# Kernel tuning notes

Measured on AMD Instinct MI355X. Metric: run time of the kernel, lower is better.

## Reference

```python
import jax, jax.numpy as jnp
import numpy as np

E = 8      # n_routed_experts (== n_local)
K = 2      # n_activated_experts (top-k)
DIM = 2048
INTER = 1408
N_SHARED = 2
STD = 0.02


def setup_inputs() -> dict:
    key = jax.random.key(0)
    ks = jax.random.split(key, 9)
    B, S = 2, 2048
    return {
        "x": jax.random.normal(ks[0], (B, S, DIM), dtype=jnp.float32),
        "gate_w": jax.random.normal(ks[1], (E, DIM), dtype=jnp.float32) * STD,
        "router_bias": jnp.zeros((E,), dtype=jnp.float32),
        "W1": jax.random.normal(ks[2], (E, DIM, INTER), dtype=jnp.float32) * STD,
        "W3": jax.random.normal(ks[3], (E, DIM, INTER), dtype=jnp.float32) * STD,
        "W2": jax.random.normal(ks[4], (E, INTER, DIM), dtype=jnp.float32) * STD,
        "sw1": jax.random.normal(ks[5], (N_SHARED * INTER, DIM), dtype=jnp.float32) * STD,
        "sw3": jax.random.normal(ks[6], (N_SHARED * INTER, DIM), dtype=jnp.float32) * STD,
        "sw2": jax.random.normal(ks[7], (DIM, N_SHARED * INTER), dtype=jnp.float32) * STD,
    }


def reference(x, gate_w, router_bias, W1, W3, W2, sw1, sw3, sw2):
    B, S, D = x.shape
    X = x.reshape(-1, D)                       # [T, D]
    T = X.shape[0]

    # ---- Router: sigmoid scores, biased top-k selection, normalized weights
    logits = jnp.einsum('td,ed->te', X, gate_w)          # [T, E] (route_scale == 1.0)
    scores = jax.nn.sigmoid(logits)
    sel = scores + router_bias[None, :]
    _, idx = jax.lax.top_k(sel, K)                       # [T, K] int indices
    w = jnp.take_along_axis(scores, idx, axis=1)         # gather true scores
    w = w / jnp.clip(jnp.sum(w, axis=-1, keepdims=True), 1e-12)

    # Dense combine matrix [T, E]: gate weight where expert selected else 0
    gate_full = jnp.zeros((T, E), dtype=w.dtype).at[jnp.arange(T)[:, None], idx].set(w)

    # ---- Expert MLPs (SwiGLU) computed per-expert, combined by routing weight
    h1 = jnp.einsum('td,edh->eth', X, W1)                # [E, T, INTER]
    h3 = jnp.einsum('td,edh->eth', X, W3)
    y = jnp.einsum('eth,ehd->etd', jax.nn.silu(h1) * h3, W2)  # [E, T, D]
    out = jnp.einsum('etd,te->td', y, gate_full)         # weighted combine

    # ---- Shared expert MLP (always on)
    shared = jnp.einsum('th,dh->td',
                        jax.nn.silu(jnp.einsum('td,hd->th', X, sw1))
                        * jnp.einsum('td,hd->th', X, sw3), sw2)
    out = out + shared
    return out.reshape(B, S, D)
```

## Files before the change

### kernel.cpp

```cpp
#include <hip/hip_runtime.h>

#define DEV __device__ __forceinline__

typedef __attribute__((ext_vector_type(8))) short short8;
typedef __attribute__((ext_vector_type(4))) float floatx4;

constexpr int Tn  = 4096;
constexpr int Dm  = 2048;
constexpr int In  = 1408;
constexpr int En  = 8;
constexpr int SIn = 2816;
constexpr int CAP = 10240;

constexpr int RT_H = (CAP / 256) * (In / 128);
constexpr int SH_H = (Tn / 256) * (SIn / 128);
constexpr int RT_O = (CAP / 256) * (Dm / 256);
constexpr int SH_O = (Tn / 256) * (Dm / 256);

DEV unsigned short f2bf(float f) {
  unsigned int u = __float_as_uint(f);
  u += 0x7FFF + ((u >> 16) & 1);
  return (unsigned short)(u >> 16);
}

DEV float bf2f(unsigned short u) {
  return __uint_as_float(((unsigned int)u) << 16);
}

DEV void stg(const char* g, char* l) {
  __builtin_amdgcn_global_load_lds(
      (const __attribute__((address_space(1))) unsigned int*)g,
      (__attribute__((address_space(3))) unsigned int*)l, 16, 0, 0);
}

DEV unsigned ldsoff(const void* p) {
  return (unsigned)(unsigned long long)(__attribute__((address_space(3))) const char*)p;
}

#define BARR()  __builtin_amdgcn_s_barrier()
#define LGKM0() do { asm volatile("s_waitcnt lgkmcnt(0)" ::: "memory"); \
                     __builtin_amdgcn_sched_barrier(0); } while (0)
#define LGKM8() asm volatile("s_waitcnt lgkmcnt(8)" ::: "memory")
#define VMC(n)  asm volatile("s_waitcnt vmcnt(" #n ")" ::: "memory")
#define PRIO(x) __builtin_amdgcn_s_setprio(x)

#define DSR(dst, addr, OFFSTR) \
  asm volatile("ds_read_b128 %0, %1 offset:" OFFSTR : "=v"(dst) : "v"(addr))

#define RDA_LO(af, a) do { \
  DSR(af[0][0], a, "0");     DSR(af[0][1], a, "1024"); \
  DSR(af[1][0], a, "2048");  DSR(af[1][1], a, "3072"); \
  DSR(af[2][0], a, "4096");  DSR(af[2][1], a, "5120"); \
  DSR(af[3][0], a, "6144");  DSR(af[3][1], a, "7168"); } while (0)
#define RDA_HI(af, a) do { \
  DSR(af[0][0], a, "8192");  DSR(af[0][1], a, "9216"); \
  DSR(af[1][0], a, "10240"); DSR(af[1][1], a, "11264"); \
  DSR(af[2][0], a, "12288"); DSR(af[2][1], a, "13312"); \
  DSR(af[3][0], a, "14336"); DSR(af[3][1], a, "15360"); } while (0)
#define RDB_LO(bf, a) do { \
  DSR(bf[0][0], a, "0");    DSR(bf[0][1], a, "1024"); \
  DSR(bf[1][0], a, "2048"); DSR(bf[1][1], a, "3072"); } while (0)
#define RDB_HI(bf, a) do { \
  DSR(bf[2][0], a, "4096"); DSR(bf[2][1], a, "5120"); \
  DSR(bf[3][0], a, "6144"); DSR(bf[3][1], a, "7168"); } while (0)


__global__ void convert_all_kernel(const float* __restrict__ x,
                                   const float* __restrict__ sw1,
                                   const float* __restrict__ sw3,
                                   const float* __restrict__ sw2,
                                   unsigned short* __restrict__ Xb,
                                   unsigned short* __restrict__ sw1b,
                                   unsigned short* __restrict__ sw3b,
                                   unsigned short* __restrict__ sw2b) {
  int y = blockIdx.y;
  const float* src; unsigned short* dst; int n4;
  if (y == 0)      { src = x;   dst = Xb;   n4 = Tn * Dm / 4; }
  else if (y == 1) { src = sw1; dst = sw1b; n4 = SIn * Dm / 4; }
  else if (y == 2) { src = sw3; dst = sw3b; n4 = SIn * Dm / 4; }
  else             { src = sw2; dst = sw2b; n4 = Dm * SIn / 4; }
  int i = blockIdx.x * 256 + threadIdx.x;
  if (i >= n4) return;
  float4 v = ((const float4*)src)[i];
  union { unsigned short u[4]; unsigned long long ll; } p;
  p.u[0] = f2bf(v.x); p.u[1] = f2bf(v.y); p.u[2] = f2bf(v.z); p.u[3] = f2bf(v.w);
  *(unsigned long long*)(dst + (long)i * 4) = p.ll;
}

__global__ void transpose_all_kernel(const float* __restrict__ W1,
                                     const float* __restrict__ W3,
                                     const float* __restrict__ W2,
                                     unsigned short* __restrict__ W1t,
                                     unsigned short* __restrict__ W3t,
                                     unsigned short* __restrict__ W2t) {
  __shared__ float tile[64][65];
  int z = blockIdx.z;
  const float* s0; unsigned short* d0; int R, C;
  if (z == 0)      { s0 = W1; d0 = W1t; R = Dm; C = In; }
  else if (z == 1) { s0 = W3; d0 = W3t; R = Dm; C = In; }
  else             { s0 = W2; d0 = W2t; R = In; C = Dm; }
  int tilesC = C >> 6;
  int tr = (blockIdx.x / tilesC) << 6;
  int tc = (blockIdx.x % tilesC) << 6;
  const float* s = s0 + (long)blockIdx.y * R * C;
  unsigned short* d = d0 + (long)blockIdx.y * R * C;
  int rr = threadIdx.x >> 4, c4 = (threadIdx.x & 15) << 2;
#pragma unroll
  for (int p = 0; p < 4; p++) {
    float4 v = *(const float4*)&s[(long)(tr + rr + 16 * p) * C + tc + c4];
    tile[rr + 16 * p][c4]     = v.x;
    tile[rr + 16 * p][c4 + 1] = v.y;
    tile[rr + 16 * p][c4 + 2] = v.z;
    tile[rr + 16 * p][c4 + 3] = v.w;
  }
  __syncthreads();
  int oc = threadIdx.x >> 5, i2 = (threadIdx.x & 31) << 1;
#pragma unroll
  for (int p = 0; p < 8; p++) {
    int j = oc + 8 * p;
    union { unsigned short u[2]; unsigned int w; } pk;
    pk.u[0] = f2bf(tile[i2][j]);
    pk.u[1] = f2bf(tile[i2 + 1][j]);
    *(unsigned int*)&d[(long)(tc + j) * R + tr + i2] = pk.w;
  }
}


__global__ void init_kernel(int* counts, int* ptok) {
  int i = blockIdx.x * 256 + threadIdx.x;
  if (i < En) counts[i] = 0;
  if (i < CAP) ptok[i] = 0;
}

__global__ void router_kernel(const float* __restrict__ X, const float* __restrict__ GW,
                              const float* __restrict__ bias,
                              int* __restrict__ route_e, float* __restrict__ route_w,
                              int* __restrict__ counts) {
  int t = blockIdx.x, lane = threadIdx.x;
  const float* xr = X + (long)t * Dm;
  double acc[En];
#pragma unroll
  for (int e = 0; e < En; e++) acc[e] = 0.0;
  for (int d = lane; d < Dm; d += 64) {
    double xv = (double)xr[d];
#pragma unroll
    for (int e = 0; e < En; e++) acc[e] += xv * (double)GW[e * Dm + d];
  }
#pragma unroll
  for (int off = 32; off > 0; off >>= 1) {
#pragma unroll
    for (int e = 0; e < En; e++) acc[e] += __shfl_down(acc[e], off);
  }
  if (lane == 0) {
    double sc[En], sel[En];
#pragma unroll
    for (int e = 0; e < En; e++) {
      sc[e] = 1.0 / (1.0 + exp(-acc[e]));
      sel[e] = sc[e] + (double)bias[e];
    }
    int i0 = 0;
#pragma unroll
    for (int e = 1; e < En; e++) if (sel[e] > sel[i0]) i0 = e;
    int i1 = (i0 == 0) ? 1 : 0;
#pragma unroll
    for (int e = 0; e < En; e++) if (e != i0 && sel[e] > sel[i1]) i1 = e;
    double s = sc[i0] + sc[i1];
    if (s < 1e-12) s = 1e-12;
    route_e[t * 2] = i0;  route_e[t * 2 + 1] = i1;
    route_w[t * 2] = (float)(sc[i0] / s);  route_w[t * 2 + 1] = (float)(sc[i1] / s);
    atomicAdd(&counts[i0], 1);  atomicAdd(&counts[i1], 1);
  }
}

__global__ void offsets_kernel(const int* __restrict__ counts,
                               int* __restrict__ offs, int* __restrict__ fill) {
  if (threadIdx.x == 0) {
    int off = 0;
    for (int e = 0; e < En; e++) {
      offs[e] = off; fill[e] = off;
      off += (counts[e] + 255) & ~255;
    }
    offs[En] = off;
  }
}

__global__ void scatter_kernel(const int* __restrict__ re, int* __restrict__ fill,
                               int* __restrict__ pt, int* __restrict__ pslot) {
  int i = blockIdx.x * 256 + threadIdx.x;
  if (i < Tn * 2) {
    int e = re[i];
    int slot = atomicAdd(&fill[e], 1);
    pt[slot] = i >> 1;
    pslot[i] = slot;
  }
}


DEV void mm16(floatx4 (&acc)[8][4], const short8 (&af)[4][2],
              const short8 (&bf)[4][2], int mq, int nq) {
#pragma unroll
  for (int i = 0; i < 4; i++)
#pragma unroll
    for (int n = 0; n < 2; n++)
#pragma unroll
      for (int kk = 0; kk < 2; kk++)
        acc[4 * mq + i][2 * nq + n] = __builtin_amdgcn_mfma_f32_16x16x32_bf16(
            af[i][kk], bf[2 * nq + n][kk], acc[4 * mq + i][2 * nq + n], 0, 0, 0);
}

DEV void chunk_rc(int c, int& rowh, int& colb) {
  rowh = ((c >> 7) << 4) | ((c >> 2) & 15);
  colb = (((c >> 6) & 1) << 6) | ((((c & 3) << 4)) ^ ((c & 32) ? 32 : 0));
}

DEV void gemm_core(char* LDS, const char* (&gA)[2][2], const char* (&gB)[2][2],
                   floatx4 (&acc)[8][4], int NT, int wm, int wn, int wv, int aswz) {
  const int bsel = (wn >> 1) * 16384 + ((wn & 1) << 13);
  const int wb = wv * 1024;
  unsigned base = ldsoff(LDS);
  unsigned aA0 = base + wm * 16384 + aswz;
  unsigned aB0 = base + 32768 + bsel + aswz;
  unsigned aA1 = aA0 + 65536, aB1 = aB0 + 65536;
  stg(gB[0][0], LDS + 32768 + wb);
  stg(gB[1][0], LDS + 32768 + 16384 + wb);
  stg(gB[0][1], LDS + 32768 + 8192 + wb);
  stg(gB[1][1], LDS + 32768 + 16384 + 8192 + wb);
  stg(gA[0][0], LDS + wb);
  stg(gA[1][0], LDS + 16384 + wb);
  stg(gA[0][1], LDS + 8192 + wb);
  stg(gA[1][1], LDS + 16384 + 8192 + wb);
  stg(gA[0][0] + 128, LDS + 65536 + wb);
  stg(gA[1][0] + 128, LDS + 65536 + 16384 + wb);
  stg(gB[0][0] + 128, LDS + 65536 + 32768 + wb);
  stg(gB[1][0] + 128, LDS + 65536 + 32768 + 16384 + wb);
  VMC(4);
  BARR();
  short8 af[4][2], bf[4][2];

  auto tile = [&](int t, int b, unsigned aA, unsigned aB) {
    char* An = LDS + ((b ^ 1) << 16);
    char* Bn = An + 32768;
    char* Ac = LDS + (b << 16);
    char* Bc = Ac + 32768;
    const int kn = (t + 1) << 7, ka = (t + 2) << 7;
    const bool s1 = (t + 1 < NT), s2 = (t + 2 < NT);
    RDA_LO(af, aA); RDB_LO(bf, aB);
    if (s1) { stg(gB[0][1] + kn, Bn + 8192 + wb);
              stg(gB[1][1] + kn, Bn + 16384 + 8192 + wb); }
    LGKM8(); BARR(); LGKM0(); PRIO(1); mm16(acc, af, bf, 0, 0); PRIO(0); BARR();
    RDB_HI(bf, aB);
    if (s1) { stg(gA[0][1] + kn, An + 8192 + wb);
              stg(gA[1][1] + kn, An + 16384 + 8192 + wb); }
    BARR(); LGKM0(); PRIO(1); mm16(acc, af, bf, 0, 1); PRIO(0); BARR();
    RDA_HI(af, aA);
    if (s2) { stg(gA[0][0] + ka, Ac + wb);
              stg(gA[1][0] + ka, Ac + 16384 + wb); }
    BARR(); LGKM0(); PRIO(1); mm16(acc, af, bf, 1, 0); PRIO(0); BARR();
    if (s2) { stg(gB[0][0] + ka, Bc + wb);
              stg(gB[1][0] + ka, Bc + 16384 + wb); }
    BARR(); LGKM0(); PRIO(1); mm16(acc, af, bf, 1, 1); PRIO(0);
    if (s2)      { VMC(4); }
    else if (s1) { VMC(0); }
    BARR();
  };
#pragma unroll 1
  for (int t2 = 0; t2 < NT; t2 += 2) {
    tile(t2, 0, aA0, aB0);
    tile(t2 + 1, 1, aA1, aB1);
  }
}


__global__ __launch_bounds__(512, 2)
void h_gemm_all(const unsigned short* __restrict__ Xb,
                const unsigned short* __restrict__ W1t,
                const unsigned short* __restrict__ W3t,
                const unsigned short* __restrict__ sw1b,
                const unsigned short* __restrict__ sw3b,
                unsigned short* __restrict__ act,
                unsigned short* __restrict__ actS,
                const int* __restrict__ ptok,
                const int* __restrict__ offs) {
  extern __shared__ char LDS[];
  int bid = blockIdx.x;
  bool routed = bid < RT_H;
  int m0, n0, Nact;
  const unsigned short *B1p, *B3p;
  unsigned short* ap;
  if (routed) {
    m0 = (bid % 40) * 256; n0 = (bid / 40) * 128;
    if (m0 >= offs[En]) return;
    int e = 0;
    while (!(m0 >= offs[e] && m0 < offs[e + 1])) e++;
    B1p = W1t + (long)e * In * Dm;
    B3p = W3t + (long)e * In * Dm;
    ap = act; Nact = In;
  } else {
    int b2 = bid - RT_H;
    m0 = (b2 % 16) * 256; n0 = (b2 / 16) * 128;
    B1p = sw1b; B3p = sw3b;
    ap = actS; Nact = SIn;
  }
  int tid = threadIdx.x, wv = tid >> 6, lane = tid & 63;
  int wm = wv >> 2, wn = wv & 3;
  int fr = lane & 15, fq = lane >> 4;
  int aswz = fr * 64 + ((fq * 16) ^ ((fr & 8) << 2));

  const char* gA[2][2]; const char* gB[2][2];
#pragma unroll
  for (int j = 0; j < 2; j++) {
    int rowh, colb;
    chunk_rc(j * 512 + tid, rowh, colb);
#pragma unroll
    for (int h = 0; h < 2; h++) {
      int grA = m0 + h * 128 + rowh;
      long ra = routed ? (long)ptok[grA] : (long)grA;
      gA[h][j] = (const char*)Xb + ra * (long)(Dm * 2) + colb;
      int rt = h * 128 + rowh;
      const unsigned short* src = ((rt >> 5) & 1) ? B3p : B1p;
      long rb = (long)n0 + ((rt >> 6) << 5) + (rt & 31);
      gB[h][j] = (const char*)src + rb * (long)(Dm * 2) + colb;
    }
  }
  floatx4 acc[8][4];
#pragma unroll
  for (int i = 0; i < 8; i++)
#pragma unroll
    for (int n = 0; n < 4; n++) acc[i][n] = (floatx4)0.0f;

  gemm_core(LDS, gA, gB, acc, Dm / 64, wm, wn, wv, aswz);

#pragma unroll
  for (int mi = 0; mi < 8; mi++)
#pragma unroll
    for (int n = 0; n < 2; n++)
#pragma unroll
      for (int r = 0; r < 4; r++) {
        int row = m0 + wm * 128 + mi * 16 + fq * 4 + r;
        int col = n0 + wn * 32 + n * 16 + fr;
        float h1 = acc[mi][n][r], h3 = acc[mi][n + 2][r];
        float v = h1 / (1.0f + __expf(-h1)) * h3;
        ap[(long)row * Nact + col] = f2bf(v);
      }
}


__global__ __launch_bounds__(512, 2)
void o_gemm_all(const unsigned short* __restrict__ act,
                const unsigned short* __restrict__ actS,
                const unsigned short* __restrict__ W2t,
                const unsigned short* __restrict__ sw2b,
                unsigned short* __restrict__ yR,
                float* __restrict__ out,
                const int* __restrict__ offs) {
  extern __shared__ char LDS[];
  int bid = blockIdx.x;
  bool routed = bid < RT_O;
  int m0, n0, lda, ldb, NT;
  const unsigned short *Apt, *Bpt;
  if (routed) {
    m0 = (bid % 40) * 256; n0 = (bid / 40) * 256;
    if (m0 >= offs[En]) return;
    int e = 0;
    while (!(m0 >= offs[e] && m0 < offs[e + 1])) e++;
    Apt = act; lda = In; Bpt = W2t + (long)e * Dm * In; ldb = In; NT = In / 64;
  } else {
    int b2 = bid - RT_O;
    m0 = (b2 % 16) * 256; n0 = (b2 / 16) * 256;
    Apt = actS; lda = SIn; Bpt = sw2b; ldb = SIn; NT = SIn / 64;
  }
  int tid = threadIdx.x, wv = tid >> 6, lane = tid & 63;
  int wm = wv >> 2, wn = wv & 3;
  int fr = lane & 15, fq = lane >> 4;
  int aswz = fr * 64 + ((fq * 16) ^ ((fr & 8) << 2));

  const char* gA[2][2]; const char* gB[2][2];
#pragma unroll
  for (int j = 0; j < 2; j++) {
    int rowh, colb;
    chunk_rc(j * 512 + tid, rowh, colb);
#pragma unroll
    for (int h = 0; h < 2; h++) {
      gA[h][j] = (const char*)Apt + (long)(m0 + h * 128 + rowh) * (lda * 2) + colb;
      gB[h][j] = (const char*)Bpt + (long)(n0 + h * 128 + rowh) * (ldb * 2) + colb;
    }
  }
  floatx4 acc[8][4];
#pragma unroll
  for (int i = 0; i < 8; i++)
#pragma unroll
    for (int n = 0; n < 4; n++) acc[i][n] = (floatx4)0.0f;

  gemm_core(LDS, gA, gB, acc, NT, wm, wn, wv, aswz);

#pragma unroll
  for (int mi = 0; mi < 8; mi++)
#pragma unroll
    for (int r = 0; r < 4; r++) {
      int row = m0 + wm * 128 + mi * 16 + fq * 4 + r;
#pragma unroll
      for (int ni = 0; ni < 4; ni++) {
        int col = n0 + wn * 64 + ni * 16 + fr;
        if (routed) yR[(long)row * Dm + col] = f2bf(acc[mi][ni][r]);
        else        out[(long)row * Dm + col] = acc[mi][ni][r];
      }
    }
}


__global__ void combine_kernel(const unsigned short* __restrict__ yR,
                               const int* __restrict__ pslot,
                               const float* __restrict__ rw,
                               float* __restrict__ out) {
  int idx = blockIdx.x * 256 + threadIdx.x;
  int t = idx >> 9, c4 = idx & 511;
  int s0 = pslot[t * 2], s1 = pslot[t * 2 + 1];
  float w0 = rw[t * 2], w1 = rw[t * 2 + 1];
  ushort4 a = ((const ushort4*)(yR + (long)s0 * Dm))[c4];
  ushort4 b = ((const ushort4*)(yR + (long)s1 * Dm))[c4];
  float4* op = (float4*)(out + (long)t * Dm) + c4;
  float4 o = *op;
  o.x += w0 * bf2f(a.x) + w1 * bf2f(b.x);
  o.y += w0 * bf2f(a.y) + w1 * bf2f(b.y);
  o.z += w0 * bf2f(a.z) + w1 * bf2f(b.z);
  o.w += w0 * bf2f(a.w) + w1 * bf2f(b.w);
  *op = o;
}


extern "C" void kernel_launch(void* const* d_in, const int* in_sizes, int n_in,
                              void* d_out, int out_size, void* d_ws, size_t ws_size,
                              hipStream_t stream) {
  const float* x    = (const float*)d_in[0];
  const float* gw   = (const float*)d_in[1];
  const float* bias = (const float*)d_in[2];
  const float* W1   = (const float*)d_in[3];
  const float* W3   = (const float*)d_in[4];
  const float* W2   = (const float*)d_in[5];
  const float* sw1  = (const float*)d_in[6];
  const float* sw3  = (const float*)d_in[7];
  const float* sw2  = (const float*)d_in[8];
  float* out = (float*)d_out;

  static bool attr_done = false;
  if (!attr_done) {
    hipFuncSetAttribute(reinterpret_cast<const void*>(h_gemm_all),
                        hipFuncAttributeMaxDynamicSharedMemorySize, 131072);
    hipFuncSetAttribute(reinterpret_cast<const void*>(o_gemm_all),
                        hipFuncAttributeMaxDynamicSharedMemorySize, 131072);
    attr_done = true;
  }

  char* p = (char*)d_ws;
  auto alloc = [&](size_t bytes) {
    char* r = p; p += (bytes + 255) & ~(size_t)255; return r;
  };
  unsigned short* Xb   = (unsigned short*)alloc((size_t)Tn * Dm * 2);
  unsigned short* W1t  = (unsigned short*)alloc((size_t)En * In * Dm * 2);
  unsigned short* W3t  = (unsigned short*)alloc((size_t)En * In * Dm * 2);
  unsigned short* W2t  = (unsigned short*)alloc((size_t)En * Dm * In * 2);
  unsigned short* sw1b = (unsigned short*)alloc((size_t)SIn * Dm * 2);
  unsigned short* sw3b = (unsigned short*)alloc((size_t)SIn * Dm * 2);
  unsigned short* sw2b = (unsigned short*)alloc((size_t)Dm * SIn * 2);
  unsigned short* act  = (unsigned short*)alloc((size_t)CAP * In * 2);
  unsigned short* actS = (unsigned short*)alloc((size_t)Tn * SIn * 2);
  unsigned short* yR   = (unsigned short*)alloc((size_t)CAP * Dm * 2);
  int*   route_e = (int*)alloc(Tn * 2 * 4);
  float* route_w = (float*)alloc(Tn * 2 * 4);
  int*   counts  = (int*)alloc(256);
  int*   offs    = (int*)alloc(256);
  int*   fill    = (int*)alloc(256);
  int*   ptok    = (int*)alloc(CAP * 4);
  int*   pslot   = (int*)alloc(Tn * 2 * 4);

  convert_all_kernel<<<dim3(Tn * Dm / 4 / 256, 4), 256, 0, stream>>>(
      x, sw1, sw3, sw2, Xb, sw1b, sw3b, sw2b);
  transpose_all_kernel<<<dim3((Dm / 64) * (In / 64), En, 3), 256, 0, stream>>>(
      W1, W3, W2, W1t, W3t, W2t);

  init_kernel<<<(CAP + 255) / 256, 256, 0, stream>>>(counts, ptok);
  router_kernel<<<Tn, 64, 0, stream>>>(x, gw, bias, route_e, route_w, counts);
  offsets_kernel<<<1, 1, 0, stream>>>(counts, offs, fill);
  scatter_kernel<<<Tn * 2 / 256, 256, 0, stream>>>(route_e, fill, ptok, pslot);

  h_gemm_all<<<RT_H + SH_H, 512, 131072, stream>>>(
      Xb, W1t, W3t, sw1b, sw3b, act, actS, ptok, offs);
  o_gemm_all<<<RT_O + SH_O, 512, 131072, stream>>>(
      act, actS, W2t, sw2b, yR, out, offs);
  combine_kernel<<<Tn * (Dm / 4) / 256, 256, 0, stream>>>(yR, pslot, route_w, out);
}
```

Before: 850.0 us.

## Fuse routed combine into down-proj epilogue via atomics, split kernels, XCD swizzle

Removes the yR bf16 intermediate and the separate combine kernel. Each routed down-projection tile now scales its results by the per-slot routing weight and atomically adds them into the fp32 output, after a shared-expert kernel has written it. The combined routed/shared GEMM launches are split into four kernels, and block indices are remapped so neighbouring tiles land on the same XCD for L2 reuse. The cost is many scattered fp32 atomicAdds, a nondeterministic summation order, and an ordering dependency on o_shared_k running before o_routed_k.

Result: slower. 915.7 us (+7.7%).

```diff
diff --git a/kernel.cpp b/kernel.cpp
--- a/kernel.cpp
+++ b/kernel.cpp
@@ -35,6 +35,11 @@
 
 DEV unsigned ldsoff(const void* p) {
   return (unsigned)(unsigned long long)(__attribute__((address_space(3))) const char*)p;
+}
+
+DEV int xcd_swz(int bid, int nwg) {
+  int cpx = nwg >> 3;
+  return (bid & 7) * cpx + (bid >> 3);
 }
 
 #define BARR()  __builtin_amdgcn_s_barrier()
@@ -126,10 +131,10 @@
 }
 
 
-__global__ void init_kernel(int* counts, int* ptok) {
+__global__ void init_kernel(int* counts, int* ptok, float* wslot) {
   int i = blockIdx.x * 256 + threadIdx.x;
   if (i < En) counts[i] = 0;
-  if (i < CAP) ptok[i] = 0;
+  if (i < CAP) { ptok[i] = 0; wslot[i] = 0.0f; }
 }
 
 __global__ void router_kernel(const float* __restrict__ X, const float* __restrict__ GW,
@@ -184,14 +189,15 @@
   }
 }
 
-__global__ void scatter_kernel(const int* __restrict__ re, int* __restrict__ fill,
-                               int* __restrict__ pt, int* __restrict__ pslot) {
+__global__ void scatter_kernel(const int* __restrict__ re, const float* __restrict__ rw,
+                               int* __restrict__ fill,
+                               int* __restrict__ pt, float* __restrict__ wslot) {
   int i = blockIdx.x * 256 + threadIdx.x;
   if (i < Tn * 2) {
     int e = re[i];
     int slot = atomicAdd(&fill[e], 1);
     pt[slot] = i >> 1;
-    pslot[i] = slot;
+    wslot[slot] = rw[i];
   }
 }
 
@@ -271,36 +277,9 @@
 }
 
 
-__global__ __launch_bounds__(512, 2)
-void h_gemm_all(const unsigned short* __restrict__ Xb,
-                const unsigned short* __restrict__ W1t,
-                const unsigned short* __restrict__ W3t,
-                const unsigned short* __restrict__ sw1b,
-                const unsigned short* __restrict__ sw3b,
-                unsigned short* __restrict__ act,
-                unsigned short* __restrict__ actS,
-                const int* __restrict__ ptok,
-                const int* __restrict__ offs) {
-  extern __shared__ char LDS[];
-  int bid = blockIdx.x;
-  bool routed = bid < RT_H;
-  int m0, n0, Nact;
-  const unsigned short *B1p, *B3p;
-  unsigned short* ap;
-  if (routed) {
-    m0 = (bid % 40) * 256; n0 = (bid / 40) * 128;
-    if (m0 >= offs[En]) return;
-    int e = 0;
-    while (!(m0 >= offs[e] && m0 < offs[e + 1])) e++;
-    B1p = W1t + (long)e * In * Dm;
-    B3p = W3t + (long)e * In * Dm;
-    ap = act; Nact = In;
-  } else {
-    int b2 = bid - RT_H;
-    m0 = (b2 % 16) * 256; n0 = (b2 / 16) * 128;
-    B1p = sw1b; B3p = sw3b;
-    ap = actS; Nact = SIn;
-  }
+DEV void h_body(const unsigned short* Xb, const unsigned short* B1p,
+                const unsigned short* B3p, unsigned short* ap, int Nact,
+                int m0, int n0, const int* ptok, bool routed, char* LDS) {
   int tid = threadIdx.x, wv = tid >> 6, lane = tid & 63;
   int wm = wv >> 2, wn = wv & 3;
   int fr = lane & 15, fq = lane >> 4;
@@ -344,31 +323,38 @@
       }
 }
 
-
 __global__ __launch_bounds__(512, 2)
-void o_gemm_all(const unsigned short* __restrict__ act,
-                const unsigned short* __restrict__ actS,
-                const unsigned short* __restrict__ W2t,
-                const unsigned short* __restrict__ sw2b,
-                unsigned short* __restrict__ yR,
-                float* __restrict__ out,
+void h_routed_k(const unsigned short* __restrict__ Xb,
+                const unsigned short* __restrict__ W1t,
+                const unsigned short* __restrict__ W3t,
+                unsigned short* __restrict__ act,
+                const int* __restrict__ ptok,
                 const int* __restrict__ offs) {
   extern __shared__ char LDS[];
-  int bid = blockIdx.x;
-  bool routed = bid < RT_O;
-  int m0, n0, lda, ldb, NT;
-  const unsigned short *Apt, *Bpt;
-  if (routed) {
-    m0 = (bid % 40) * 256; n0 = (bid / 40) * 256;
-    if (m0 >= offs[En]) return;
-    int e = 0;
-    while (!(m0 >= offs[e] && m0 < offs[e + 1])) e++;
-    Apt = act; lda = In; Bpt = W2t + (long)e * Dm * In; ldb = In; NT = In / 64;
-  } else {
-    int b2 = bid - RT_O;
-    m0 = (b2 % 16) * 256; n0 = (b2 / 16) * 256;
-    Apt = actS; lda = SIn; Bpt = sw2b; ldb = SIn; NT = SIn / 64;
-  }
+  int bid = xcd_swz(blockIdx.x, RT_H);
+  int m0 = (bid % 40) * 256, n0 = (bid / 40) * 128;
+  if (m0 >= offs[En]) return;
+  int e = 0;
+  while (!(m0 >= offs[e] && m0 < offs[e + 1])) e++;
+  h_body(Xb, W1t + (long)e * In * Dm, W3t + (long)e * In * Dm,
+         act, In, m0, n0, ptok, true, LDS);
+}
+
+__global__ __launch_bounds__(512, 2)
+void h_shared_k(const unsigned short* __restrict__ Xb,
+                const unsigned short* __restrict__ sw1b,
+                const unsigned short* __restrict__ sw3b,
+                unsigned short* __restrict__ actS) {
+  extern __shared__ char LDS[];
+  int bid = xcd_swz(blockIdx.x, SH_H);
+  int m0 = (bid % 16) * 256, n0 = (bid / 16) * 128;
+  h_body(Xb, sw1b, sw3b, actS, SIn, m0, n0, nullptr, false, LDS);
+}
+
+
+DEV void o_core(const unsigned short* Apt, const unsigned short* Bpt,
+                int lda, int ldb, int NT, int m0, int n0,
+                floatx4 (&acc)[8][4], char* LDS) {
   int tid = threadIdx.x, wv = tid >> 6, lane = tid & 63;
   int wm = wv >> 2, wn = wv & 3;
   int fr = lane & 15, fq = lane >> 4;
@@ -385,46 +371,74 @@
       gB[h][j] = (const char*)Bpt + (long)(n0 + h * 128 + rowh) * (ldb * 2) + colb;
     }
   }
+#pragma unroll
+  for (int i = 0; i < 8; i++)
+#pragma unroll
+    for (int n = 0; n < 4; n++) acc[i][n] = (floatx4)0.0f;
+
+  gemm_core(LDS, gA, gB, acc, NT, wm, wn, wv, aswz);
+}
+
+__global__ __launch_bounds__(512, 2)
+void o_routed_k(const unsigned short* __restrict__ act,
+                const unsigned short* __restrict__ W2t,
+                float* __restrict__ out,
+                const int* __restrict__ ptok,
+                const float* __restrict__ wslot,
+                const int* __restrict__ offs) {
+  extern __shared__ char LDS[];
+  int bid = xcd_swz(blockIdx.x, RT_O);
+  int m0 = (bid % 40) * 256, n0 = (bid / 40) * 256;
+  if (m0 >= offs[En]) return;
+  int e = 0;
+  while (!(m0 >= offs[e] && m0 < offs[e + 1])) e++;
   floatx4 acc[8][4];
-#pragma unroll
-  for (int i = 0; i < 8; i++)
-#pragma unroll
-    for (int n = 0; n < 4; n++) acc[i][n] = (floatx4)0.0f;
-
-  gemm_core(LDS, gA, gB, acc, NT, wm, wn, wv, aswz);
-
+  o_core(act, W2t + (long)e * Dm * In, In, In, In / 64, m0, n0, acc, LDS);
+
+  int lane = threadIdx.x & 63, wv = threadIdx.x >> 6;
+  int wm = wv >> 2, wn = wv & 3;
+  int fr = lane & 15, fq = lane >> 4;
 #pragma unroll
   for (int mi = 0; mi < 8; mi++)
 #pragma unroll
     for (int r = 0; r < 4; r++) {
       int row = m0 + wm * 128 + mi * 16 + fq * 4 + r;
+      int tok = ptok[row];
+      float w = wslot[row];
+      if (w != 0.0f) {
+#pragma unroll
+        for (int ni = 0; ni < 4; ni++) {
+          int col = n0 + wn * 64 + ni * 16 + fr;
+          atomicAdd(&out[(long)tok * Dm + col], w * acc[mi][ni][r]);
+        }
+      }
+    }
+}
+
+__global__ __launch_bounds__(512, 2)
+void o_shared_k(const unsigned short* __restrict__ actS,
+                const unsigned short* __restrict__ sw2b,
+                float* __restrict__ out) {
+  extern __shared__ char LDS[];
+  int bid = xcd_swz(blockIdx.x, SH_O);
+  int m0 = (bid % 16) * 256, n0 = (bid / 16) * 256;
+  floatx4 acc[8][4];
+  o_core(actS, sw2b, SIn, SIn, SIn / 64, m0, n0, acc, LDS);
+
+  int lane = threadIdx.x & 63, wv = threadIdx.x >> 6;
+  int wm = wv >> 2, wn = wv & 3;
+  int fr = lane & 15, fq = lane >> 4;
+#pragma unroll
+  for (int mi = 0; mi < 8; mi++)
+#pragma unroll
+    for (int r = 0; r < 4; r++) {
+      int row = m0 + wm * 128 + mi * 16 + fq * 4 + r;
 #pragma unroll
       for (int ni = 0; ni < 4; ni++) {
         int col = n0 + wn * 64 + ni * 16 + fr;
-        if (routed) yR[(long)row * Dm + col] = f2bf(acc[mi][ni][r]);
-        else        out[(long)row * Dm + col] = acc[mi][ni][r];
+        out[(long)row * Dm + col] = acc[mi][ni][r];
       }
     }
-}
-
-
-__global__ void combine_kernel(const unsigned short* __restrict__ yR,
-                               const int* __restrict__ pslot,
-                               const float* __restrict__ rw,
-                               float* __restrict__ out) {
-  int idx = blockIdx.x * 256 + threadIdx.x;
-  int t = idx >> 9, c4 = idx & 511;
-  int s0 = pslot[t * 2], s1 = pslot[t * 2 + 1];
-  float w0 = rw[t * 2], w1 = rw[t * 2 + 1];
-  ushort4 a = ((const ushort4*)(yR + (long)s0 * Dm))[c4];
-  ushort4 b = ((const ushort4*)(yR + (long)s1 * Dm))[c4];
-  float4* op = (float4*)(out + (long)t * Dm) + c4;
-  float4 o = *op;
-  o.x += w0 * bf2f(a.x) + w1 * bf2f(b.x);
-  o.y += w0 * bf2f(a.y) + w1 * bf2f(b.y);
-  o.z += w0 * bf2f(a.z) + w1 * bf2f(b.z);
-  o.w += w0 * bf2f(a.w) + w1 * bf2f(b.w);
-  *op = o;
 }
 
 
@@ -444,9 +458,13 @@
 
   static bool attr_done = false;
   if (!attr_done) {
-    hipFuncSetAttribute(reinterpret_cast<const void*>(h_gemm_all),
+    hipFuncSetAttribute(reinterpret_cast<const void*>(h_routed_k),
                         hipFuncAttributeMaxDynamicSharedMemorySize, 131072);
-    hipFuncSetAttribute(reinterpret_cast<const void*>(o_gemm_all),
+    hipFuncSetAttribute(reinterpret_cast<const void*>(h_shared_k),
+                        hipFuncAttributeMaxDynamicSharedMemorySize, 131072);
+    hipFuncSetAttribute(reinterpret_cast<const void*>(o_routed_k),
+                        hipFuncAttributeMaxDynamicSharedMemorySize, 131072);
+    hipFuncSetAttribute(reinterpret_cast<const void*>(o_shared_k),
                         hipFuncAttributeMaxDynamicSharedMemorySize, 131072);
     attr_done = true;
   }
@@ -464,28 +482,26 @@
   unsigned short* sw2b = (unsigned short*)alloc((size_t)Dm * SIn * 2);
   unsigned short* act  = (unsigned short*)alloc((size_t)CAP * In * 2);
   unsigned short* actS = (unsigned short*)alloc((size_t)Tn * SIn * 2);
-  unsigned short* yR   = (unsigned short*)alloc((size_t)CAP * Dm * 2);
   int*   route_e = (int*)alloc(Tn * 2 * 4);
   float* route_w = (float*)alloc(Tn * 2 * 4);
   int*   counts  = (int*)alloc(256);
   int*   offs    = (int*)alloc(256);
   int*   fill    = (int*)alloc(256);
   int*   ptok    = (int*)alloc(CAP * 4);
-  int*   pslot   = (int*)alloc(Tn * 2 * 4);
+  float* wslot   = (float*)alloc(CAP * 4);
 
   convert_all_kernel<<<dim3(Tn * Dm / 4 / 256, 4), 256, 0, stream>>>(
       x, sw1, sw3, sw2, Xb, sw1b, sw3b, sw2b);
   transpose_all_kernel<<<dim3((Dm / 64) * (In / 64), En, 3), 256, 0, stream>>>(
       W1, W3, W2, W1t, W3t, W2t);
 
-  init_kernel<<<(CAP + 255) / 256, 256, 0, stream>>>(counts, ptok);
+  init_kernel<<<(CAP + 255) / 256, 256, 0, stream>>>(counts, ptok, wslot);
   router_kernel<<<Tn, 64, 0, stream>>>(x, gw, bias, route_e, route_w, counts);
   offsets_kernel<<<1, 1, 0, stream>>>(counts, offs, fill);
-  scatter_kernel<<<Tn * 2 / 256, 256, 0, stream>>>(route_e, fill, ptok, pslot);
-
-  h_gemm_all<<<RT_H + SH_H, 512, 131072, stream>>>(
-      Xb, W1t, W3t, sw1b, sw3b, act, actS, ptok, offs);
-  o_gemm_all<<<RT_O + SH_O, 512, 131072, stream>>>(
-      act, actS, W2t, sw2b, yR, out, offs);
-  combine_kernel<<<Tn * (Dm / 4) / 256, 256, 0, stream>>>(yR, pslot, route_w, out);
-}
+  scatter_kernel<<<Tn * 2 / 256, 256, 0, stream>>>(route_e, route_w, fill, ptok, wslot);
+
+  h_shared_k<<<SH_H, 512, 131072, stream>>>(Xb, sw1b, sw3b, actS);
+  h_routed_k<<<RT_H, 512, 131072, stream>>>(Xb, W1t, W3t, act, ptok, offs);
+  o_shared_k<<<SH_O, 512, 131072, stream>>>(actS, sw2b, out);
+  o_routed_k<<<RT_O, 512, 131072, stream>>>(act, W2t, out, ptok, wslot, offs);
+}
```

## Convert expert GEMMs to persistent kernels iterating over live tiles

Applied to the files above, without the earlier changes.

Replaces the fixed oversized grids, in which routed blocks past the used capacity exit early, with persistent kernels of 256 blocks that loop over only the valid routed tiles plus the shared tiles. The tile index now decodes the M dimension by the actual number of used row blocks. This removes launch and scheduling overhead for dead blocks and packs the work onto one wave of CTAs. In exchange, launch bounds drop to 1 block per CU, which can change register allocation and occupancy, and load balance now depends on a static stride.

Result: faster. 832.5 us (-2.1%).

```diff
diff --git a/kernel.cpp b/kernel.cpp
--- a/kernel.cpp
+++ b/kernel.cpp
@@ -12,10 +12,9 @@
 constexpr int SIn = 2816;
 constexpr int CAP = 10240;
 
-constexpr int RT_H = (CAP / 256) * (In / 128);
 constexpr int SH_H = (Tn / 256) * (SIn / 128);
-constexpr int RT_O = (CAP / 256) * (Dm / 256);
 constexpr int SH_O = (Tn / 256) * (Dm / 256);
+constexpr int NBLK = 256;
 
 DEV unsigned short f2bf(float f) {
   unsigned int u = __float_as_uint(f);
@@ -271,36 +270,9 @@
 }
 
 
-__global__ __launch_bounds__(512, 2)
-void h_gemm_all(const unsigned short* __restrict__ Xb,
-                const unsigned short* __restrict__ W1t,
-                const unsigned short* __restrict__ W3t,
-                const unsigned short* __restrict__ sw1b,
-                const unsigned short* __restrict__ sw3b,
-                unsigned short* __restrict__ act,
-                unsigned short* __restrict__ actS,
-                const int* __restrict__ ptok,
-                const int* __restrict__ offs) {
-  extern __shared__ char LDS[];
-  int bid = blockIdx.x;
-  bool routed = bid < RT_H;
-  int m0, n0, Nact;
-  const unsigned short *B1p, *B3p;
-  unsigned short* ap;
-  if (routed) {
-    m0 = (bid % 40) * 256; n0 = (bid / 40) * 128;
-    if (m0 >= offs[En]) return;
-    int e = 0;
-    while (!(m0 >= offs[e] && m0 < offs[e + 1])) e++;
-    B1p = W1t + (long)e * In * Dm;
-    B3p = W3t + (long)e * In * Dm;
-    ap = act; Nact = In;
-  } else {
-    int b2 = bid - RT_H;
-    m0 = (b2 % 16) * 256; n0 = (b2 / 16) * 128;
-    B1p = sw1b; B3p = sw3b;
-    ap = actS; Nact = SIn;
-  }
+DEV void h_body(const unsigned short* Xb, const unsigned short* B1p,
+                const unsigned short* B3p, unsigned short* ap, int Nact,
+                int m0, int n0, const int* ptok, bool routed, char* LDS) {
   int tid = threadIdx.x, wv = tid >> 6, lane = tid & 63;
   int wm = wv >> 2, wn = wv & 3;
   int fr = lane & 15, fq = lane >> 4;
@@ -344,31 +316,40 @@
       }
 }
 
-
-__global__ __launch_bounds__(512, 2)
-void o_gemm_all(const unsigned short* __restrict__ act,
-                const unsigned short* __restrict__ actS,
-                const unsigned short* __restrict__ W2t,
-                const unsigned short* __restrict__ sw2b,
-                unsigned short* __restrict__ yR,
-                float* __restrict__ out,
-                const int* __restrict__ offs) {
+__global__ __launch_bounds__(512, 1)
+void h_all(const unsigned short* __restrict__ Xb,
+           const unsigned short* __restrict__ W1t,
+           const unsigned short* __restrict__ W3t,
+           const unsigned short* __restrict__ sw1b,
+           const unsigned short* __restrict__ sw3b,
+           unsigned short* __restrict__ act,
+           unsigned short* __restrict__ actS,
+           const int* __restrict__ ptok,
+           const int* __restrict__ offs) {
   extern __shared__ char LDS[];
-  int bid = blockIdx.x;
-  bool routed = bid < RT_O;
-  int m0, n0, lda, ldb, NT;
-  const unsigned short *Apt, *Bpt;
-  if (routed) {
-    m0 = (bid % 40) * 256; n0 = (bid / 40) * 256;
-    if (m0 >= offs[En]) return;
-    int e = 0;
-    while (!(m0 >= offs[e] && m0 < offs[e + 1])) e++;
-    Apt = act; lda = In; Bpt = W2t + (long)e * Dm * In; ldb = In; NT = In / 64;
-  } else {
-    int b2 = bid - RT_O;
-    m0 = (b2 % 16) * 256; n0 = (b2 / 16) * 256;
-    Apt = actS; lda = SIn; Bpt = sw2b; ldb = SIn; NT = SIn / 64;
-  }
+  const int Mr = offs[En] >> 8;
+  const int RT = Mr * (In / 128);
+  const int TT = RT + SH_H;
+#pragma unroll 1
+  for (int t = blockIdx.x; t < TT; t += NBLK) {
+    if (t < RT) {
+      int m0 = (t % Mr) * 256, n0 = (t / Mr) * 128;
+      int e = 0;
+      while (!(m0 >= offs[e] && m0 < offs[e + 1])) e++;
+      h_body(Xb, W1t + (long)e * In * Dm, W3t + (long)e * In * Dm,
+             act, In, m0, n0, ptok, true, LDS);
+    } else {
+      int u = t - RT;
+      int m0 = (u & 15) * 256, n0 = (u >> 4) * 128;
+      h_body(Xb, sw1b, sw3b, actS, SIn, m0, n0, nullptr, false, LDS);
+    }
+  }
+}
+
+
+DEV void o_core(const unsigned short* Apt, const unsigned short* Bpt,
+                int lda, int ldb, int NT, int m0, int n0,
+                floatx4 (&acc)[8][4], char* LDS) {
   int tid = threadIdx.x, wv = tid >> 6, lane = tid & 63;
   int wm = wv >> 2, wn = wv & 3;
   int fr = lane & 15, fq = lane >> 4;
@@ -385,26 +366,65 @@
       gB[h][j] = (const char*)Bpt + (long)(n0 + h * 128 + rowh) * (ldb * 2) + colb;
     }
   }
-  floatx4 acc[8][4];
 #pragma unroll
   for (int i = 0; i < 8; i++)
 #pragma unroll
     for (int n = 0; n < 4; n++) acc[i][n] = (floatx4)0.0f;
 
   gemm_core(LDS, gA, gB, acc, NT, wm, wn, wv, aswz);
-
-#pragma unroll
-  for (int mi = 0; mi < 8; mi++)
-#pragma unroll
-    for (int r = 0; r < 4; r++) {
-      int row = m0 + wm * 128 + mi * 16 + fq * 4 + r;
-#pragma unroll
-      for (int ni = 0; ni < 4; ni++) {
-        int col = n0 + wn * 64 + ni * 16 + fr;
-        if (routed) yR[(long)row * Dm + col] = f2bf(acc[mi][ni][r]);
-        else        out[(long)row * Dm + col] = acc[mi][ni][r];
-      }
+}
+
+__global__ __launch_bounds__(512, 1)
+void o_all(const unsigned short* __restrict__ act,
+           const unsigned short* __restrict__ actS,
+           const unsigned short* __restrict__ W2t,
+           const unsigned short* __restrict__ sw2b,
+           unsigned short* __restrict__ yR,
+           float* __restrict__ out,
+           const int* __restrict__ offs) {
+  extern __shared__ char LDS[];
+  const int Mr = offs[En] >> 8;
+  const int RT = Mr * (Dm / 256);
+  const int TT = RT + SH_O;
+  int lane = threadIdx.x & 63, wv = threadIdx.x >> 6;
+  int wm = wv >> 2, wn = wv & 3;
+  int fr = lane & 15, fq = lane >> 4;
+#pragma unroll 1
+  for (int t = blockIdx.x; t < TT; t += NBLK) {
+    floatx4 acc[8][4];
+    if (t < RT) {
+      int m0 = (t % Mr) * 256, n0 = (t / Mr) * 256;
+      int e = 0;
+      while (!(m0 >= offs[e] && m0 < offs[e + 1])) e++;
+      o_core(act, W2t + (long)e * Dm * In, In, In, In / 64, m0, n0, acc, LDS);
+#pragma unroll
+      for (int mi = 0; mi < 8; mi++)
+#pragma unroll
+        for (int r = 0; r < 4; r++) {
+          int row = m0 + wm * 128 + mi * 16 + fq * 4 + r;
+#pragma unroll
+          for (int ni = 0; ni < 4; ni++) {
+            int col = n0 + wn * 64 + ni * 16 + fr;
+            yR[(long)row * Dm + col] = f2bf(acc[mi][ni][r]);
+          }
+        }
+    } else {
+      int u = t - RT;
+      int m0 = (u & 15) * 256, n0 = (u >> 4) * 256;
+      o_core(actS, sw2b, SIn, SIn, SIn / 64, m0, n0, acc, LDS);
+#pragma unroll
+      for (int mi = 0; mi < 8; mi++)
+#pragma unroll
+        for (int r = 0; r < 4; r++) {
+          int row = m0 + wm * 128 + mi * 16 + fq * 4 + r;
+#pragma unroll
+          for (int ni = 0; ni < 4; ni++) {
+            int col = n0 + wn * 64 + ni * 16 + fr;
+            out[(long)row * Dm + col] = acc[mi][ni][r];
+          }
+        }
     }
+  }
 }
 
 
@@ -444,9 +464,9 @@
 
   static bool attr_done = false;
   if (!attr_done) {
-    hipFuncSetAttribute(reinterpret_cast<const void*>(h_gemm_all),
+    hipFuncSetAttribute(reinterpret_cast<const void*>(h_all),
                         hipFuncAttributeMaxDynamicSharedMemorySize, 131072);
-    hipFuncSetAttribute(reinterpret_cast<const void*>(o_gemm_all),
+    hipFuncSetAttribute(reinterpret_cast<const void*>(o_all),
                         hipFuncAttributeMaxDynamicSharedMemorySize, 131072);
     attr_done = true;
   }
@@ -483,9 +503,7 @@
   offsets_kernel<<<1, 1, 0, stream>>>(counts, offs, fill);
   scatter_kernel<<<Tn * 2 / 256, 256, 0, stream>>>(route_e, fill, ptok, pslot);
 
-  h_gemm_all<<<RT_H + SH_H, 512, 131072, stream>>>(
-      Xb, W1t, W3t, sw1b, sw3b, act, actS, ptok, offs);
-  o_gemm_all<<<RT_O + SH_O, 512, 131072, stream>>>(
-      act, actS, W2t, sw2b, yR, out, offs);
+  h_all<<<NBLK, 512, 131072, stream>>>(Xb, W1t, W3t, sw1b, sw3b, act, actS, ptok, offs);
+  o_all<<<NBLK, 512, 131072, stream>>>(act, actS, W2t, sw2b, yR, out, offs);
   combine_kernel<<<Tn * (Dm / 4) / 256, 256, 0, stream>>>(yR, pslot, route_w, out);
 }
```
